# Optimization experiments

Hardware: AMD Instinct MI355X
Metric: run time of the kernel (lower is better)

## Reference

```python
import jax, jax.numpy as jnp
import numpy as np

V, D, H, L, S_MAX, FF = 32000, 1024, 16, 6, 1024, 4096
HD = D // H
EPS = 1e-5

def _ln(x, g, b):
    mu = jnp.mean(x, axis=-1, keepdims=True)
    var = jnp.mean((x - mu) ** 2, axis=-1, keepdims=True)
    return (x - mu) * jax.lax.rsqrt(var + EPS) * g + b

def setup_inputs() -> dict:
    key = jax.random.key(0)
    ks = jax.random.split(key, 12)
    std = 0.02
    d = {}
    d['x'] = jax.random.randint(ks[0], (2, 1024), 0, V)
    d['tok_emb'] = std * jax.random.normal(ks[1], (V, D), jnp.float32)
    d['pos_emb'] = std * jax.random.normal(ks[2], (S_MAX, D), jnp.float32)
    d['ln1_g'] = jnp.ones((L, D)); d['ln1_b'] = jnp.zeros((L, D))
    d['qkv_w'] = std * jax.random.normal(ks[3], (L, 3 * D, D), jnp.float32)
    d['qkv_b'] = jnp.zeros((L, 3 * D))
    d['proj_w'] = std * jax.random.normal(ks[4], (L, D, D), jnp.float32)
    d['proj_b'] = jnp.zeros((L, D))
    d['ln2_g'] = jnp.ones((L, D)); d['ln2_b'] = jnp.zeros((L, D))
    d['fc1_w'] = std * jax.random.normal(ks[5], (L, FF, D), jnp.float32)
    d['fc1_b'] = jnp.zeros((L, FF))
    d['fc2_w'] = std * jax.random.normal(ks[6], (L, D, FF), jnp.float32)
    d['fc2_b'] = jnp.zeros((L, D))
    d['lnf_g'] = jnp.ones((D,)); d['lnf_b'] = jnp.zeros((D,))
    d['head_w'] = std * jax.random.normal(ks[7], (V, D), jnp.float32)
    return d

def _gpt(x, tok_emb, pos_emb, ln1_g, ln1_b, qkv_w, qkv_b, proj_w, proj_b,
         ln2_g, ln2_b, fc1_w, fc1_b, fc2_w, fc2_b, lnf_g, lnf_b, head_w):
    B, S = x.shape
    h = tok_emb[x] + pos_emb[:S][None]  # (B,S,D)
    scale = HD ** -0.5
    causal = jnp.tril(jnp.ones((S, S), bool))
    neg_inf = jnp.finfo(h.dtype).min

    def block(h, p):
        l1g, l1b, qw, qb, pw, pb, l2g, l2b, f1w, f1b, f2w, f2b = p
        xn = _ln(h, l1g, l1b)
        qkv = xn @ qw.T + qb  # (B,S,3D)
        qkv = qkv.reshape(B, S, 3, H, HD).transpose(2, 0, 3, 1, 4)  # (3,B,H,S,HD)
        q, k, v = qkv[0], qkv[1], qkv[2]
        scores = jnp.einsum('bhqd,bhkd->bhqk', q, k) * scale
        scores = jnp.where(causal, scores, neg_inf)
        attn = jax.nn.softmax(scores, axis=-1)
        o = jnp.einsum('bhqk,bhkd->bhqd', attn, v)
        o = o.transpose(0, 2, 1, 3).reshape(B, S, D)
        h = h + (o @ pw.T + pb)
        xn = _ln(h, l2g, l2b)
        ff = jax.nn.gelu(xn @ f1w.T + f1b, approximate=False) @ f2w.T + f2b
        return h + ff, None

    params = (ln1_g, ln1_b, qkv_w, qkv_b, proj_w, proj_b,
              ln2_g, ln2_b, fc1_w, fc1_b, fc2_w, fc2_b)
    h, _ = jax.lax.scan(block, h, params)
    h = _ln(h, lnf_g, lnf_b)
    return h @ head_w.T  # (B,S,V)

def reference(x, tok_emb, pos_emb, ln1_g, ln1_b, qkv_w, qkv_b, proj_w, proj_b,
              ln2_g, ln2_b, fc1_w, fc1_b, fc2_w, fc2_b, lnf_g, lnf_b, head_w):
    return _gpt(x, tok_emb, pos_emb, ln1_g, ln1_b, qkv_w, qkv_b, proj_w, proj_b,
                ln2_g, ln2_b, fc1_w, fc1_b, fc2_w, fc2_b, lnf_g, lnf_b, head_w)
```

## Files before the change

kernel.cpp:

```cpp
#include <hip/hip_runtime.h>

typedef unsigned short u16;
typedef unsigned int   u32;
typedef __bf16 bf16x8 __attribute__((ext_vector_type(8)));
typedef float  f32x4  __attribute__((ext_vector_type(4)));

#define DEV __device__ __forceinline__

DEV u16 f2bf(float f) {
    u32 u = __builtin_bit_cast(u32, f);
    u32 r = u + 0x7FFFu + ((u >> 16) & 1u);
    return (u16)(r >> 16);
}

DEV void gload16(const void* g, void* l) {
    __builtin_amdgcn_global_load_lds((const __attribute__((address_space(1))) void*)g,
                                     (__attribute__((address_space(3))) void*)l, 16, 0, 0);
}

DEV int xcd_swz(int bid, int nwg) {
    int q = nwg >> 3, r = nwg & 7;
    int xcd = bid & 7, idx = bid >> 3;
    return (xcd < r ? xcd * (q + 1) : r * (q + 1) + (xcd - r) * q) + idx;
}

DEV int swz(int p) {
    int m = (((p >> 7) & 1) << 6) | (((p >> 9) & 1) << 5) | (((p >> 8) & 1) << 4);
    return p ^ m;
}

__global__ void cvt_k(const float* __restrict__ src, u16* __restrict__ dst, int n4) {
    int i = blockIdx.x * blockDim.x + threadIdx.x;
    int stride = gridDim.x * blockDim.x;
    for (; i < n4; i += stride) {
        float4 v = ((const float4*)src)[i];
        ushort4 u;
        u.x = f2bf(v.x); u.y = f2bf(v.y); u.z = f2bf(v.z); u.w = f2bf(v.w);
        ((ushort4*)dst)[i] = u;
    }
}

__global__ void cvt4_k(const float* __restrict__ s0, const float* __restrict__ s1,
                       const float* __restrict__ s2, const float* __restrict__ s3,
                       u16* __restrict__ dst, int n0, int n1, int n2, int n3) {
    int i = blockIdx.x * blockDim.x + threadIdx.x;
    int stride = gridDim.x * blockDim.x;
    int t0 = n0, t1 = t0 + n1, t2 = t1 + n2, t3 = t2 + n3;
    for (; i < t3; i += stride) {
        const float* s; int j;
        if (i < t0)      { s = s0; j = i; }
        else if (i < t1) { s = s1; j = i - t0; }
        else if (i < t2) { s = s2; j = i - t1; }
        else             { s = s3; j = i - t2; }
        float4 v = ((const float4*)s)[j];
        ushort4 u;
        u.x = f2bf(v.x); u.y = f2bf(v.y); u.z = f2bf(v.z); u.w = f2bf(v.w);
        ((ushort4*)dst)[i] = u;
    }
}

DEV void ln_store(float4 v, const float* __restrict__ g, const float* __restrict__ b,
                  u16* __restrict__ out, int row, int t) {
    float s = v.x + v.y + v.z + v.w;
    float s2 = v.x * v.x + v.y * v.y + v.z * v.z + v.w * v.w;
    #pragma unroll
    for (int msk = 1; msk < 64; msk <<= 1) {
        s  += __shfl_xor(s, msk);
        s2 += __shfl_xor(s2, msk);
    }
    __shared__ float ps[4], ps2[4];
    if ((t & 63) == 0) { ps[t >> 6] = s; ps2[t >> 6] = s2; }
    __syncthreads();
    s = ps[0] + ps[1] + ps[2] + ps[3];
    s2 = ps2[0] + ps2[1] + ps2[2] + ps2[3];
    float mu = s * (1.0f / 1024.0f);
    float var = s2 * (1.0f / 1024.0f) - mu * mu;
    float rstd = rsqrtf(var + 1e-5f);
    float4 gg = ((const float4*)g)[t];
    float4 bb = ((const float4*)b)[t];
    ushort4 o;
    o.x = f2bf((v.x - mu) * rstd * gg.x + bb.x);
    o.y = f2bf((v.y - mu) * rstd * gg.y + bb.y);
    o.z = f2bf((v.z - mu) * rstd * gg.z + bb.z);
    o.w = f2bf((v.w - mu) * rstd * gg.w + bb.w);
    ((ushort4*)out)[(size_t)row * 256 + t] = o;
}

__global__ void ln_k(const float* __restrict__ in, const float* __restrict__ g,
                     const float* __restrict__ b, u16* __restrict__ out) {
    int row = blockIdx.x;
    int t = threadIdx.x;
    float4 v = ((const float4*)(in + (size_t)row * 1024))[t];
    ln_store(v, g, b, out, row, t);
}

__global__ void embed_ln_k(const int* __restrict__ x, const float* __restrict__ te,
                           const float* __restrict__ pe, float* __restrict__ h,
                           const float* __restrict__ g, const float* __restrict__ b,
                           u16* __restrict__ xn) {
    int row = blockIdx.x;
    int t = threadIdx.x;
    int tok = x[row];
    int s = row & 1023;
    float4 a = ((const float4*)(te + (size_t)tok * 1024))[t];
    float4 p = ((const float4*)(pe + (size_t)s * 1024))[t];
    a.x += p.x; a.y += p.y; a.z += p.z; a.w += p.w;
    ((float4*)(h + (size_t)row * 1024))[t] = a;
    ln_store(a, g, b, xn, row, t);
}

__global__ void fuse2ln_k(const float* __restrict__ p0, const float* __restrict__ p1,
                          const float* __restrict__ bias, float* __restrict__ h,
                          const float* __restrict__ g, const float* __restrict__ b,
                          u16* __restrict__ xn) {
    int row = blockIdx.x;
    int t = threadIdx.x;
    size_t idx = (size_t)row * 256 + t;
    float4 a = ((const float4*)p0)[idx];
    float4 bb = ((const float4*)p1)[idx];
    float4 c = ((const float4*)bias)[t];
    float4 v = ((const float4*)h)[idx];
    v.x += a.x + bb.x + c.x;
    v.y += a.y + bb.y + c.y;
    v.z += a.z + bb.z + c.z;
    v.w += a.w + bb.w + c.w;
    ((float4*)h)[idx] = v;
    ln_store(v, g, b, xn, row, t);
}

template<int PH>
DEV void phase_mma(const bf16x8 (&af)[2][2], const bf16x8 (&bfr)[4][2], f32x4 (&acc)[8][4]) {
    __builtin_amdgcn_s_barrier();
    asm volatile("s_waitcnt lgkmcnt(0)" ::: "memory");
    __builtin_amdgcn_sched_barrier(0);
    __builtin_amdgcn_s_setprio(1);
    #pragma unroll
    for (int ms = 0; ms < 2; ++ms)
        #pragma unroll
        for (int nj = 0; nj < 4; ++nj)
            #pragma unroll
            for (int kk = 0; kk < 2; ++kk)
                acc[PH * 2 + ms][nj] = __builtin_amdgcn_mfma_f32_16x16x32_bf16(
                    af[ms][kk], bfr[nj][kk], acc[PH * 2 + ms][nj], 0, 0, 0);
    __builtin_amdgcn_s_setprio(0);
}

template<int PH>
DEV void read_afrags(const char* Ab, int arow, int fr, int fq, bf16x8 (&af)[2][2]) {
    #pragma unroll
    for (int ms = 0; ms < 2; ++ms)
        #pragma unroll
        for (int kk = 0; kk < 2; ++kk) {
            int lin = (arow + (PH * 2 + ms) * 16 + fr) * 128 + kk * 64 + fq * 16;
            af[ms][kk] = *(const bf16x8*)(Ab + swz(lin));
        }
}

template<int BIAS, int OUTBF>
__global__ __launch_bounds__(512, 2)
void gemm8p(const u16* __restrict__ A, const u16* __restrict__ Bw,
            const float* __restrict__ bias,
            float* __restrict__ outf, u16* __restrict__ outb,
            int M, int N, int K) {
    __shared__ char lds[131072];
    char* ldsA = lds;
    char* ldsB = lds + 65536;
    const int t = threadIdx.x;
    const int w = t >> 6, l = t & 63;
    const int fr = l & 15, fq = l >> 4;
    const int wm = w >> 2, wn = w & 3;

    int bid = blockIdx.y * gridDim.x + blockIdx.x;
    int swzb = xcd_swz(bid, gridDim.x * gridDim.y);
    const int m0 = (swzb % gridDim.x) * 256;
    const int n0 = (swzb / gridDim.x) * 256;
    const int nt = K >> 6;
    const int arow = wm * 128;

    const u16* Asrc = A + (size_t)m0 * K;
    const u16* Bsrc = Bw + (size_t)n0 * K;

    size_t o00, o01, o10, o11;
    {
        int p;
        p = 0 * 16384 + 0 * 8192 + t * 16; o00 = (size_t)(p >> 7) * K + ((swz(p) & 127) >> 1);
        p = 0 * 16384 + 1 * 8192 + t * 16; o01 = (size_t)(p >> 7) * K + ((swz(p) & 127) >> 1);
        p = 1 * 16384 + 0 * 8192 + t * 16; o10 = (size_t)(p >> 7) * K + ((swz(p) & 127) >> 1);
        p = 1 * 16384 + 1 * 8192 + t * 16; o11 = (size_t)(p >> 7) * K + ((swz(p) & 127) >> 1);
    }
    const int wb = w * 1024;

    gload16(Asrc + o00, ldsA + wb);
    gload16(Asrc + o01, ldsA + 8192 + wb);
    gload16(Asrc + o10, ldsA + 16384 + wb);
    gload16(Asrc + o11, ldsA + 16384 + 8192 + wb);
    gload16(Bsrc + o00, ldsB + wb);
    gload16(Bsrc + o01, ldsB + 8192 + wb);
    gload16(Bsrc + o10, ldsB + 16384 + wb);
    gload16(Bsrc + o11, ldsB + 16384 + 8192 + wb);
    gload16(Bsrc + o00 + 64, ldsB + 32768 + wb);
    gload16(Bsrc + o01 + 64, ldsB + 32768 + 8192 + wb);
    gload16(Bsrc + o10 + 64, ldsB + 32768 + 16384 + wb);
    gload16(Bsrc + o11 + 64, ldsB + 32768 + 16384 + 8192 + wb);
    asm volatile("s_waitcnt vmcnt(4)" ::: "memory");
    __builtin_amdgcn_s_barrier();
    __builtin_amdgcn_sched_barrier(0);

    f32x4 acc[8][4] = {};

    for (int T = 0; T < nt; ++T) {
        const char* Ab = ldsA + (T & 1) * 32768;
        const char* Bb = ldsB + (T & 1) * 32768;
        char* Anx = ldsA + ((T + 1) & 1) * 32768;
        char* Bnx = ldsB + (T & 1) * 32768;
        const bool stA = (T + 1 < nt), stB = (T + 2 < nt);
        const size_t kA = (size_t)(T + 1) * 64, kB = (size_t)(T + 2) * 64;

        bf16x8 bfr[4][2], af[2][2];

        #pragma unroll
        for (int nj = 0; nj < 4; ++nj)
            #pragma unroll
            for (int kk = 0; kk < 2; ++kk) {
                int lin = (wn * 64 + nj * 16 + fr) * 128 + kk * 64 + fq * 16;
                bfr[nj][kk] = *(const bf16x8*)(Bb + swz(lin));
            }
        read_afrags<0>(Ab, arow, fr, fq, af);
        if (stA) {
            gload16(Asrc + o00 + kA, Anx + wb);
            gload16(Asrc + o01 + kA, Anx + 8192 + wb);
        }
        phase_mma<0>(af, bfr, acc);
        __builtin_amdgcn_s_barrier();

        read_afrags<1>(Ab, arow, fr, fq, af);
        if (stA) {
            gload16(Asrc + o10 + kA, Anx + 16384 + wb);
            gload16(Asrc + o11 + kA, Anx + 16384 + 8192 + wb);
        }
        phase_mma<1>(af, bfr, acc);
        __builtin_amdgcn_s_barrier();

        read_afrags<2>(Ab, arow, fr, fq, af);
        if (stB) {
            gload16(Bsrc + o00 + kB, Bnx + wb);
            gload16(Bsrc + o01 + kB, Bnx + 8192 + wb);
        }
        phase_mma<2>(af, bfr, acc);
        __builtin_amdgcn_s_barrier();

        read_afrags<3>(Ab, arow, fr, fq, af);
        if (stB) {
            gload16(Bsrc + o10 + kB, Bnx + 16384 + wb);
            gload16(Bsrc + o11 + kB, Bnx + 16384 + 8192 + wb);
        }
        phase_mma<3>(af, bfr, acc);
        if (stB)      asm volatile("s_waitcnt vmcnt(4)" ::: "memory");
        else if (stA) asm volatile("s_waitcnt vmcnt(0)" ::: "memory");
        __builtin_amdgcn_s_barrier();
        __builtin_amdgcn_sched_barrier(0);
    }

    #pragma unroll
    for (int mi = 0; mi < 8; ++mi) {
        #pragma unroll
        for (int nj = 0; nj < 4; ++nj) {
            #pragma unroll
            for (int r = 0; r < 4; ++r) {
                int row = m0 + wm * 128 + mi * 16 + fq * 4 + r;
                int col = n0 + wn * 64 + nj * 16 + fr;
                float v = acc[mi][nj][r];
                if (BIAS) v += bias[col];
                if (OUTBF) outb[(size_t)row * N + col] = f2bf(v);
                else       outf[(size_t)row * N + col] = v;
            }
        }
    }
}

template<int BIAS, int GELU_, int OUTBF, int SPLITK>
__global__ __launch_bounds__(512, 2)
void gemm4p(const u16* __restrict__ A, const u16* __restrict__ Bw,
            const float* __restrict__ bias,
            float* __restrict__ outf, u16* __restrict__ outb,
            int M, int N, int K) {
    __shared__ char lds[65536];
    char* ldsA = lds;
    char* ldsB = lds + 32768;
    const int t = threadIdx.x;
    const int w = t >> 6, l = t & 63;
    const int fr = l & 15, fq = l >> 4;
    const int wm = w >> 2, wn = w & 3;

    int bid = blockIdx.y * gridDim.x + blockIdx.x;
    int swzb = xcd_swz(bid, gridDim.x * gridDim.y);
    const int m0 = (swzb % gridDim.x) * 128;
    const int n0 = (swzb / gridDim.x) * 128;

    int kbase = 0, Keff = K;
    if (SPLITK) { Keff = K >> 1; kbase = blockIdx.z * Keff; }
    const int nt = Keff >> 6;

    const u16* Asrc = A + (size_t)m0 * K + kbase;
    const u16* Bsrc = Bw + (size_t)n0 * K + kbase;

    size_t o0, o1;
    {
        int p = t * 16;        o0 = (size_t)(p >> 7) * K + ((swz(p) & 127) >> 1);
        p = 8192 + t * 16;     o1 = (size_t)(p >> 7) * K + ((swz(p) & 127) >> 1);
    }
    const int wb = w * 1024;

    gload16(Asrc + o0, ldsA + wb);
    gload16(Asrc + o1, ldsA + 8192 + wb);
    gload16(Bsrc + o0, ldsB + wb);
    gload16(Bsrc + o1, ldsB + 8192 + wb);
    gload16(Bsrc + o0 + 64, ldsB + 16384 + wb);
    gload16(Bsrc + o1 + 64, ldsB + 16384 + 8192 + wb);
    asm volatile("s_waitcnt vmcnt(2)" ::: "memory");
    __builtin_amdgcn_s_barrier();
    __builtin_amdgcn_sched_barrier(0);

    f32x4 acc[4][2] = {};

    for (int T = 0; T < nt; ++T) {
        const char* Ab = ldsA + (T & 1) * 16384;
        const char* Bb = ldsB + (T & 1) * 16384;
        char* Anx = ldsA + ((T + 1) & 1) * 16384;
        char* Bnx = ldsB + (T & 1) * 16384;
        const bool stA = (T + 1 < nt), stB = (T + 2 < nt);
        const size_t kA = (size_t)(T + 1) * 64, kB = (size_t)(T + 2) * 64;

        bf16x8 bfr[2][2], af[2][2];

        #pragma unroll
        for (int nj = 0; nj < 2; ++nj)
            #pragma unroll
            for (int kk = 0; kk < 2; ++kk) {
                int lin = (wn * 32 + nj * 16 + fr) * 128 + kk * 64 + fq * 16;
                bfr[nj][kk] = *(const bf16x8*)(Bb + swz(lin));
            }
        #pragma unroll
        for (int ms = 0; ms < 2; ++ms)
            #pragma unroll
            for (int kk = 0; kk < 2; ++kk) {
                int lin = (wm * 64 + ms * 16 + fr) * 128 + kk * 64 + fq * 16;
                af[ms][kk] = *(const bf16x8*)(Ab + swz(lin));
            }
        if (stA) {
            gload16(Asrc + o0 + kA, Anx + wb);
            gload16(Asrc + o1 + kA, Anx + 8192 + wb);
        }
        __builtin_amdgcn_s_barrier();
        asm volatile("s_waitcnt lgkmcnt(0)" ::: "memory");
        __builtin_amdgcn_sched_barrier(0);
        __builtin_amdgcn_s_setprio(1);
        #pragma unroll
        for (int ms = 0; ms < 2; ++ms)
            #pragma unroll
            for (int nj = 0; nj < 2; ++nj)
                #pragma unroll
                for (int kk = 0; kk < 2; ++kk)
                    acc[ms][nj] = __builtin_amdgcn_mfma_f32_16x16x32_bf16(
                        af[ms][kk], bfr[nj][kk], acc[ms][nj], 0, 0, 0);
        __builtin_amdgcn_s_setprio(0);
        __builtin_amdgcn_s_barrier();

        #pragma unroll
        for (int ms = 0; ms < 2; ++ms)
            #pragma unroll
            for (int kk = 0; kk < 2; ++kk) {
                int lin = (wm * 64 + (2 + ms) * 16 + fr) * 128 + kk * 64 + fq * 16;
                af[ms][kk] = *(const bf16x8*)(Ab + swz(lin));
            }
        if (stB) {
            gload16(Bsrc + o0 + kB, Bnx + wb);
            gload16(Bsrc + o1 + kB, Bnx + 8192 + wb);
        }
        __builtin_amdgcn_s_barrier();
        asm volatile("s_waitcnt lgkmcnt(0)" ::: "memory");
        __builtin_amdgcn_sched_barrier(0);
        __builtin_amdgcn_s_setprio(1);
        #pragma unroll
        for (int ms = 0; ms < 2; ++ms)
            #pragma unroll
            for (int nj = 0; nj < 2; ++nj)
                #pragma unroll
                for (int kk = 0; kk < 2; ++kk)
                    acc[2 + ms][nj] = __builtin_amdgcn_mfma_f32_16x16x32_bf16(
                        af[ms][kk], bfr[nj][kk], acc[2 + ms][nj], 0, 0, 0);
        __builtin_amdgcn_s_setprio(0);
        if (stB)      asm volatile("s_waitcnt vmcnt(2)" ::: "memory");
        else if (stA) asm volatile("s_waitcnt vmcnt(0)" ::: "memory");
        __builtin_amdgcn_s_barrier();
        __builtin_amdgcn_sched_barrier(0);
    }

    float* op = outf;
    if (SPLITK) op = outf + (size_t)blockIdx.z * M * N;

    #pragma unroll
    for (int mi = 0; mi < 4; ++mi) {
        #pragma unroll
        for (int nj = 0; nj < 2; ++nj) {
            #pragma unroll
            for (int r = 0; r < 4; ++r) {
                int row = m0 + wm * 64 + mi * 16 + fq * 4 + r;
                int col = n0 + wn * 32 + nj * 16 + fr;
                float v = acc[mi][nj][r];
                if (BIAS) v += bias[col];
                if (GELU_) v = 0.5f * v * (1.0f + erff(v * 0.70710678118f));
                if (OUTBF) outb[(size_t)row * N + col] = f2bf(v);
                else       op[(size_t)row * N + col] = v;
            }
        }
    }
}

template<int BM, int BN, int BIAS, int GELU_, int RES, int OUTBF, int SPLITK>
__global__ void gemm_db(const u16* __restrict__ A, const u16* __restrict__ Bw,
                        const float* __restrict__ bias, const float* __restrict__ res,
                        float* __restrict__ outf, u16* __restrict__ outb,
                        int M, int N, int K) {
    constexpr int MR = BM / 32;
    constexpr int NR = BN / 32;
    constexpr int AL = BM / 64;
    constexpr int BL = BN / 64;
    __shared__ u16 lA[2][BM * 32];
    __shared__ u16 lB[2][BN * 32];
    const int t = threadIdx.x;
    const int w = t >> 6, l = t & 63;

    int bid = blockIdx.y * gridDim.x + blockIdx.x;
    int swzb = xcd_swz(bid, gridDim.x * gridDim.y);
    const int m0 = (swzb % gridDim.x) * BM;
    const int n0 = (swzb / gridDim.x) * BN;

    int kbase = 0, Keff = K;
    if (SPLITK) { Keff = K >> 1; kbase = blockIdx.z * Keff; }
    const int nt = Keff >> 5;

    const int wr = (w >> 1) * (BM / 2), wc = (w & 1) * (BN / 2);
    const int fr = l & 15, fq = l >> 4;
    const int g0 = w * 64 + l;

    const int srow = g0 >> 2, scol = (g0 & 3) * 8;

    f32x4 acc[MR][NR] = {};

    #pragma unroll
    for (int i = 0; i < AL; ++i)
        gload16(A + (size_t)(m0 + srow + i * 64) * K + kbase + scol, lA[0] + (srow + i * 64) * 32 + scol);
    #pragma unroll
    for (int i = 0; i < BL; ++i)
        gload16(Bw + (size_t)(n0 + srow + i * 64) * K + kbase + scol, lB[0] + (srow + i * 64) * 32 + scol);
    __syncthreads();

    for (int T = 0; T < nt; ++T) {
        const int cur = T & 1, nxt = cur ^ 1;
        if (T + 1 < nt) {
            const int kk = kbase + (T + 1) * 32;
            #pragma unroll
            for (int i = 0; i < AL; ++i)
                gload16(A + (size_t)(m0 + srow + i * 64) * K + kk + scol, lA[nxt] + (srow + i * 64) * 32 + scol);
            #pragma unroll
            for (int i = 0; i < BL; ++i)
                gload16(Bw + (size_t)(n0 + srow + i * 64) * K + kk + scol, lB[nxt] + (srow + i * 64) * 32 + scol);
        }
        bf16x8 af[MR], bfv[NR];
        #pragma unroll
        for (int mi = 0; mi < MR; ++mi)
            af[mi] = *(const bf16x8*)(lA[cur] + (wr + mi * 16 + fr) * 32 + fq * 8);
        #pragma unroll
        for (int ni = 0; ni < NR; ++ni)
            bfv[ni] = *(const bf16x8*)(lB[cur] + (wc + ni * 16 + fr) * 32 + fq * 8);
        #pragma unroll
        for (int mi = 0; mi < MR; ++mi)
            #pragma unroll
            for (int ni = 0; ni < NR; ++ni)
                acc[mi][ni] = __builtin_amdgcn_mfma_f32_16x16x32_bf16(af[mi], bfv[ni], acc[mi][ni], 0, 0, 0);
        __syncthreads();
    }

    float* op = outf;
    if (SPLITK) op = outf + (size_t)blockIdx.z * M * N;

    #pragma unroll
    for (int mi = 0; mi < MR; ++mi) {
        #pragma unroll
        for (int ni = 0; ni < NR; ++ni) {
            #pragma unroll
            for (int r = 0; r < 4; ++r) {
                int row = m0 + wr + mi * 16 + fq * 4 + r;
                int col = n0 + wc + ni * 16 + fr;
                float v = acc[mi][ni][r];
                if (BIAS) v += bias[col];
                if (GELU_) v = 0.5f * v * (1.0f + erff(v * 0.70710678118f));
                if (RES) v += res[(size_t)row * N + col];
                if (OUTBF) outb[(size_t)row * N + col] = f2bf(v);
                else       op[(size_t)row * N + col] = v;
            }
        }
    }
}

__global__ __launch_bounds__(512, 2)
void attn_k(const u16* __restrict__ qkv, u16* __restrict__ o) {
    __shared__ u16 lK[2][64 * 64];
    __shared__ u16 lV[2][64 * 64];
    __shared__ u16 lP[8 * 16 * 64];
    const int t = threadIdx.x;
    const int w = t >> 6, l = t & 63;
    const int fr = l & 15, fq = l >> 4;

    int swzb = xcd_swz(blockIdx.x, gridDim.x);
    const int qb = 7 - (swzb & 7);
    const int hh = (swzb >> 3) & 15;
    const int b  = swzb >> 7;
    const int q0 = qb * 128;
    const int qw = q0 + w * 16;

    const u16* srcK;
    {
        int p = t * 16;
        int L = swz(p);
        srcK = qkv + ((size_t)(b * 1024) + (L >> 7)) * 3072 + 1024 + hh * 64 + ((L & 127) >> 1);
    }

    const int kvp = (t & 31) * 2;
    const int vd0 = (t >> 5) * 4;
    const u16* srcV = qkv + (size_t)(b * 1024) * 3072 + 2048 + hh * 64 + vd0;

    bf16x8 qf[2];
    {
        size_t base = ((size_t)(b * 1024) + qw + fr) * 3072 + hh * 64;
        qf[0] = *(const bf16x8*)(qkv + base + fq * 8);
        qf[1] = *(const bf16x8*)(qkv + base + 32 + fq * 8);
    }

    float m_run[4], l_run[4];
    f32x4 acc_o[4] = {};
    #pragma unroll
    for (int r = 0; r < 4; ++r) { m_run[r] = -__builtin_inff(); l_run[r] = 0.0f; }

    uint2 gv0 = *(const uint2*)(srcV + (size_t)kvp * 3072);
    uint2 gv1 = *(const uint2*)(srcV + (size_t)(kvp + 1) * 3072);
    gload16(srcK, (char*)lK[0] + w * 1024);
    #pragma unroll
    for (int j = 0; j < 4; ++j) {
        u32 lo = (j < 2) ? gv0.x : gv0.y;
        u32 hi = (j < 2) ? gv1.x : gv1.y;
        lo = (j & 1) ? (lo >> 16) : (lo & 0xffffu);
        hi = (j & 1) ? (hi >> 16) : (hi & 0xffffu);
        u32 word = lo | (hi << 16);
        int pv = (vd0 + j) * 128 + kvp * 2;
        *(u32*)((char*)lV[0] + swz(pv)) = word;
    }

    const int kv_end = q0 + 128;
    int cur = 0;
    for (int kv0 = 0; kv0 < kv_end; kv0 += 64, cur ^= 1) {
        __syncthreads();
        const int nxt = cur ^ 1;
        const bool more = (kv0 + 64 < kv_end);
        if (more) {
            gload16(srcK + (size_t)(kv0 + 64) * 3072, (char*)lK[nxt] + w * 1024);
            gv0 = *(const uint2*)(srcV + (size_t)(kv0 + 64 + kvp) * 3072);
            gv1 = *(const uint2*)(srcV + (size_t)(kv0 + 64 + kvp + 1) * 3072);
        }

        const bool active = (kv0 <= qw + 15);
        if (active) {
            f32x4 accs[4] = {};
            #pragma unroll
            for (int nt = 0; nt < 4; ++nt) {
                #pragma unroll
                for (int ks = 0; ks < 2; ++ks) {
                    int pk = ((nt * 16 + fr) * 64 + ks * 32 + fq * 8) * 2;
                    bf16x8 kf = *(const bf16x8*)((const char*)lK[cur] + swz(pk));
                    accs[nt] = __builtin_amdgcn_mfma_f32_16x16x32_bf16(qf[ks], kf, accs[nt], 0, 0, 0);
                }
            }

            float p[4][4], mx[4], rs[4];
            #pragma unroll
            for (int r = 0; r < 4; ++r) {
                int qg = qw + fq * 4 + r;
                float m = -__builtin_inff();
                #pragma unroll
                for (int nt = 0; nt < 4; ++nt) {
                    int kvg = kv0 + nt * 16 + fr;
                    float s = (kvg <= qg) ? accs[nt][r] * 0.125f : -__builtin_inff();
                    p[nt][r] = s;
                    m = fmaxf(m, s);
                }
                mx[r] = m;
            }
            #pragma unroll
            for (int msk = 1; msk < 16; msk <<= 1) {
                #pragma unroll
                for (int r = 0; r < 4; ++r) mx[r] = fmaxf(mx[r], __shfl_xor(mx[r], msk));
            }

            bool need = false;
            #pragma unroll
            for (int r = 0; r < 4; ++r) need |= (mx[r] > m_run[r] + 8.0f);
            if (__any(need)) {
                float mnew[4], alpha[4];
                #pragma unroll
                for (int r = 0; r < 4; ++r) {
                    mnew[r] = fmaxf(m_run[r], mx[r]);
                    alpha[r] = __expf(m_run[r] - mnew[r]);
                    float s = 0.0f;
                    #pragma unroll
                    for (int nt = 0; nt < 4; ++nt) {
                        float pv = __expf(p[nt][r] - mnew[r]);
                        p[nt][r] = pv;
                        s += pv;
                    }
                    rs[r] = s;
                }
                #pragma unroll
                for (int msk = 1; msk < 16; msk <<= 1) {
                    #pragma unroll
                    for (int r = 0; r < 4; ++r) rs[r] += __shfl_xor(rs[r], msk);
                }
                #pragma unroll
                for (int r = 0; r < 4; ++r) {
                    l_run[r] = l_run[r] * alpha[r] + rs[r];
                    m_run[r] = mnew[r];
                }
                #pragma unroll
                for (int nt = 0; nt < 4; ++nt)
                    #pragma unroll
                    for (int r = 0; r < 4; ++r) acc_o[nt][r] *= alpha[r];
            } else {
                #pragma unroll
                for (int r = 0; r < 4; ++r) {
                    float s = 0.0f;
                    #pragma unroll
                    for (int nt = 0; nt < 4; ++nt) {
                        float pv = __expf(p[nt][r] - m_run[r]);
                        p[nt][r] = pv;
                        s += pv;
                    }
                    rs[r] = s;
                }
                #pragma unroll
                for (int msk = 1; msk < 16; msk <<= 1) {
                    #pragma unroll
                    for (int r = 0; r < 4; ++r) rs[r] += __shfl_xor(rs[r], msk);
                }
                #pragma unroll
                for (int r = 0; r < 4; ++r) l_run[r] += rs[r];
            }

            #pragma unroll
            for (int nt = 0; nt < 4; ++nt)
                #pragma unroll
                for (int r = 0; r < 4; ++r) {
                    int pp = (w * 1024 + (fq * 4 + r) * 64 + nt * 16 + fr) * 2;
                    *(u16*)((char*)lP + swz(pp)) = f2bf(p[nt][r]);
                }

            bf16x8 pa[2];
            #pragma unroll
            for (int ks = 0; ks < 2; ++ks) {
                int ppr = (w * 1024 + fr * 64 + ks * 32 + fq * 8) * 2;
                pa[ks] = *(const bf16x8*)((const char*)lP + swz(ppr));
            }
            #pragma unroll
            for (int nt = 0; nt < 4; ++nt) {
                #pragma unroll
                for (int ks = 0; ks < 2; ++ks) {
                    int pvr = ((nt * 16 + fr) * 64 + ks * 32 + fq * 8) * 2;
                    bf16x8 vf = *(const bf16x8*)((const char*)lV[cur] + swz(pvr));
                    acc_o[nt] = __builtin_amdgcn_mfma_f32_16x16x32_bf16(pa[ks], vf, acc_o[nt], 0, 0, 0);
                }
            }
        }

        if (more) {
            #pragma unroll
            for (int j = 0; j < 4; ++j) {
                u32 lo = (j < 2) ? gv0.x : gv0.y;
                u32 hi = (j < 2) ? gv1.x : gv1.y;
                lo = (j & 1) ? (lo >> 16) : (lo & 0xffffu);
                hi = (j & 1) ? (hi >> 16) : (hi & 0xffffu);
                u32 word = lo | (hi << 16);
                int pv = (vd0 + j) * 128 + kvp * 2;
                *(u32*)((char*)lV[nxt] + swz(pv)) = word;
            }
        }
    }

    #pragma unroll
    for (int nt = 0; nt < 4; ++nt) {
        #pragma unroll
        for (int r = 0; r < 4; ++r) {
            int qg = qw + fq * 4 + r;
            int d = nt * 16 + fr;
            float ov = acc_o[nt][r] / l_run[r];
            o[((size_t)(b * 1024) + qg) * 1024 + hh * 64 + d] = f2bf(ov);
        }
    }
}

extern "C" void kernel_launch(void* const* d_in, const int* in_sizes, int n_in,
                              void* d_out, int out_size, void* d_ws, size_t ws_size,
                              hipStream_t stream) {
    const int*   x       = (const int*)  d_in[0];
    const float* tok_emb = (const float*)d_in[1];
    const float* pos_emb = (const float*)d_in[2];
    const float* ln1_g   = (const float*)d_in[3];
    const float* ln1_b   = (const float*)d_in[4];
    const float* qkv_w   = (const float*)d_in[5];
    const float* qkv_b   = (const float*)d_in[6];
    const float* proj_w  = (const float*)d_in[7];
    const float* proj_b  = (const float*)d_in[8];
    const float* ln2_g   = (const float*)d_in[9];
    const float* ln2_b   = (const float*)d_in[10];
    const float* fc1_w   = (const float*)d_in[11];
    const float* fc1_b   = (const float*)d_in[12];
    const float* fc2_w   = (const float*)d_in[13];
    const float* fc2_b   = (const float*)d_in[14];
    const float* lnf_g   = (const float*)d_in[15];
    const float* lnf_b   = (const float*)d_in[16];
    const float* head_w  = (const float*)d_in[17];
    float* out = (float*)d_out;

    char* ws = (char*)d_ws;
    float* h   = (float*)(ws + 0);
    u16*   xn  = (u16*)(ws + 8388608);
    u16*   qkv = (u16*)(ws + 12582912);
    u16*   ob  = (u16*)(ws + 25165824);
    u16*   ff  = (u16*)(ws + 29360128);
    u16*   wq  = (u16*)(ws + 46137344);
    float* pbuf = (float*)(ws + 12582912);

    u16* wqkv = wq;
    u16* wproj = wqkv + 3072 * 1024;
    u16* wfc1  = wproj + 1024 * 1024;
    u16* wfc2  = wfc1 + 4096 * 1024;

    const int M = 2048;

    embed_ln_k<<<dim3(2048), 256, 0, stream>>>(x, tok_emb, pos_emb, h, ln1_g, ln1_b, xn);

    for (int lyr = 0; lyr < 6; ++lyr) {
        cvt4_k<<<dim3(2048), 256, 0, stream>>>(
            qkv_w + (size_t)lyr * 3072 * 1024, proj_w + (size_t)lyr * 1024 * 1024,
            fc1_w + (size_t)lyr * 4096 * 1024, fc2_w + (size_t)lyr * 1024 * 4096,
            wq, 3072 * 256, 1024 * 256, 4096 * 256, 4096 * 256);
        gemm4p<1, 0, 1, 0><<<dim3(16, 24), 512, 0, stream>>>(
            xn, wqkv, qkv_b + lyr * 3072, nullptr, qkv, M, 3072, 1024);
        attn_k<<<dim3(256), 512, 0, stream>>>(qkv, ob);
        gemm_db<64, 64, 1, 0, 1, 0, 0><<<dim3(32, 16), 256, 0, stream>>>(
            ob, wproj, proj_b + lyr * 1024, h, h, nullptr, M, 1024, 1024);
        ln_k<<<dim3(2048), 256, 0, stream>>>(h, ln2_g + lyr * 1024, ln2_b + lyr * 1024, xn);
        gemm4p<1, 1, 1, 0><<<dim3(16, 32), 512, 0, stream>>>(
            xn, wfc1, fc1_b + lyr * 4096, nullptr, ff, M, 4096, 1024);
        gemm4p<0, 0, 0, 1><<<dim3(16, 8, 2), 512, 0, stream>>>(
            ff, wfc2, nullptr, pbuf, nullptr, M, 1024, 4096);
        const float* g = (lyr < 5) ? (ln1_g + (lyr + 1) * 1024) : lnf_g;
        const float* b = (lyr < 5) ? (ln1_b + (lyr + 1) * 1024) : lnf_b;
        fuse2ln_k<<<dim3(2048), 256, 0, stream>>>(
            pbuf, pbuf + (size_t)M * 1024, fc2_b + lyr * 1024, h, g, b, xn);
    }

    cvt_k<<<dim3(2048), 256, 0, stream>>>(head_w, wq, 32000 * 1024 / 4);
    gemm8p<0, 0><<<dim3(8, 125), 512, 0, stream>>>(
        xn, wq, nullptr, out, nullptr, M, 32000, 1024);
}
```

Measured before the change: 1.193 ms.

## Halve K tile of LM-head GEMM to 32 to shrink LDS footprint

Rewrites the 256x256 LM-head GEMM kernel to step K by 32 instead of 64, with a new swizzle for 64-byte rows, halving LDS use from 128KB to 64KB. Each iteration now runs in two phases of 16 MFMAs instead of four phases of 8. The smaller LDS footprint may let more workgroups reside per CU, but the kernel now has twice as many iterations and barriers per K and less compute per barrier.

```diff
diff --git a/kernel.cpp b/kernel.cpp
--- a/kernel.cpp
+++ b/kernel.cpp
@@ -26,6 +26,11 @@
 
 DEV int swz(int p) {
     int m = (((p >> 7) & 1) << 6) | (((p >> 9) & 1) << 5) | (((p >> 8) & 1) << 4);
+    return p ^ m;
+}
+
+DEV int swz32(int p) {
+    int m = (((p >> 7) & 1) << 5) | (((p >> 8) & 1) << 4);
     return p ^ m;
 }
 
@@ -128,43 +133,15 @@
     ln_store(v, g, b, xn, row, t);
 }
 
-template<int PH>
-DEV void phase_mma(const bf16x8 (&af)[2][2], const bf16x8 (&bfr)[4][2], f32x4 (&acc)[8][4]) {
-    __builtin_amdgcn_s_barrier();
-    asm volatile("s_waitcnt lgkmcnt(0)" ::: "memory");
-    __builtin_amdgcn_sched_barrier(0);
-    __builtin_amdgcn_s_setprio(1);
-    #pragma unroll
-    for (int ms = 0; ms < 2; ++ms)
-        #pragma unroll
-        for (int nj = 0; nj < 4; ++nj)
-            #pragma unroll
-            for (int kk = 0; kk < 2; ++kk)
-                acc[PH * 2 + ms][nj] = __builtin_amdgcn_mfma_f32_16x16x32_bf16(
-                    af[ms][kk], bfr[nj][kk], acc[PH * 2 + ms][nj], 0, 0, 0);
-    __builtin_amdgcn_s_setprio(0);
-}
-
-template<int PH>
-DEV void read_afrags(const char* Ab, int arow, int fr, int fq, bf16x8 (&af)[2][2]) {
-    #pragma unroll
-    for (int ms = 0; ms < 2; ++ms)
-        #pragma unroll
-        for (int kk = 0; kk < 2; ++kk) {
-            int lin = (arow + (PH * 2 + ms) * 16 + fr) * 128 + kk * 64 + fq * 16;
-            af[ms][kk] = *(const bf16x8*)(Ab + swz(lin));
-        }
-}
-
 template<int BIAS, int OUTBF>
 __global__ __launch_bounds__(512, 2)
-void gemm8p(const u16* __restrict__ A, const u16* __restrict__ Bw,
-            const float* __restrict__ bias,
-            float* __restrict__ outf, u16* __restrict__ outb,
-            int M, int N, int K) {
-    __shared__ char lds[131072];
+void gemm8p32(const u16* __restrict__ A, const u16* __restrict__ Bw,
+              const float* __restrict__ bias,
+              float* __restrict__ outf, u16* __restrict__ outb,
+              int M, int N, int K) {
+    __shared__ char lds[65536];
     char* ldsA = lds;
-    char* ldsB = lds + 65536;
+    char* ldsB = lds + 32768;
     const int t = threadIdx.x;
     const int w = t >> 6, l = t & 63;
     const int fr = l & 15, fq = l >> 4;
@@ -174,88 +151,89 @@
     int swzb = xcd_swz(bid, gridDim.x * gridDim.y);
     const int m0 = (swzb % gridDim.x) * 256;
     const int n0 = (swzb / gridDim.x) * 256;
-    const int nt = K >> 6;
+    const int nt = K >> 5;
     const int arow = wm * 128;
 
     const u16* Asrc = A + (size_t)m0 * K;
     const u16* Bsrc = Bw + (size_t)n0 * K;
 
-    size_t o00, o01, o10, o11;
+    size_t o0, o1;
     {
-        int p;
-        p = 0 * 16384 + 0 * 8192 + t * 16; o00 = (size_t)(p >> 7) * K + ((swz(p) & 127) >> 1);
-        p = 0 * 16384 + 1 * 8192 + t * 16; o01 = (size_t)(p >> 7) * K + ((swz(p) & 127) >> 1);
-        p = 1 * 16384 + 0 * 8192 + t * 16; o10 = (size_t)(p >> 7) * K + ((swz(p) & 127) >> 1);
-        p = 1 * 16384 + 1 * 8192 + t * 16; o11 = (size_t)(p >> 7) * K + ((swz(p) & 127) >> 1);
+        int p = t * 16;        o0 = (size_t)(p >> 6) * K + ((swz32(p) & 63) >> 1);
+        p = 8192 + t * 16;     o1 = (size_t)(p >> 6) * K + ((swz32(p) & 63) >> 1);
     }
     const int wb = w * 1024;
 
-    gload16(Asrc + o00, ldsA + wb);
-    gload16(Asrc + o01, ldsA + 8192 + wb);
-    gload16(Asrc + o10, ldsA + 16384 + wb);
-    gload16(Asrc + o11, ldsA + 16384 + 8192 + wb);
-    gload16(Bsrc + o00, ldsB + wb);
-    gload16(Bsrc + o01, ldsB + 8192 + wb);
-    gload16(Bsrc + o10, ldsB + 16384 + wb);
-    gload16(Bsrc + o11, ldsB + 16384 + 8192 + wb);
-    gload16(Bsrc + o00 + 64, ldsB + 32768 + wb);
-    gload16(Bsrc + o01 + 64, ldsB + 32768 + 8192 + wb);
-    gload16(Bsrc + o10 + 64, ldsB + 32768 + 16384 + wb);
-    gload16(Bsrc + o11 + 64, ldsB + 32768 + 16384 + 8192 + wb);
-    asm volatile("s_waitcnt vmcnt(4)" ::: "memory");
+    gload16(Asrc + o0, ldsA + wb);
+    gload16(Asrc + o1, ldsA + 8192 + wb);
+    gload16(Bsrc + o0, ldsB + wb);
+    gload16(Bsrc + o1, ldsB + 8192 + wb);
+    gload16(Bsrc + o0 + 32, ldsB + 16384 + wb);
+    gload16(Bsrc + o1 + 32, ldsB + 16384 + 8192 + wb);
+    asm volatile("s_waitcnt vmcnt(2)" ::: "memory");
     __builtin_amdgcn_s_barrier();
     __builtin_amdgcn_sched_barrier(0);
 
     f32x4 acc[8][4] = {};
 
     for (int T = 0; T < nt; ++T) {
-        const char* Ab = ldsA + (T & 1) * 32768;
-        const char* Bb = ldsB + (T & 1) * 32768;
-        char* Anx = ldsA + ((T + 1) & 1) * 32768;
-        char* Bnx = ldsB + (T & 1) * 32768;
+        const char* Ab = ldsA + (T & 1) * 16384;
+        const char* Bb = ldsB + (T & 1) * 16384;
+        char* Anx = ldsA + ((T + 1) & 1) * 16384;
+        char* Bnx = ldsB + (T & 1) * 16384;
         const bool stA = (T + 1 < nt), stB = (T + 2 < nt);
-        const size_t kA = (size_t)(T + 1) * 64, kB = (size_t)(T + 2) * 64;
-
-        bf16x8 bfr[4][2], af[2][2];
-
-        #pragma unroll
-        for (int nj = 0; nj < 4; ++nj)
-            #pragma unroll
-            for (int kk = 0; kk < 2; ++kk) {
-                int lin = (wn * 64 + nj * 16 + fr) * 128 + kk * 64 + fq * 16;
-                bfr[nj][kk] = *(const bf16x8*)(Bb + swz(lin));
-            }
-        read_afrags<0>(Ab, arow, fr, fq, af);
+        const size_t kA = (size_t)(T + 1) * 32, kB = (size_t)(T + 2) * 32;
+
+        bf16x8 bfr[4], af[4];
+
+        #pragma unroll
+        for (int nj = 0; nj < 4; ++nj) {
+            int lin = (wn * 64 + nj * 16 + fr) * 64 + fq * 16;
+            bfr[nj] = *(const bf16x8*)(Bb + swz32(lin));
+        }
+        #pragma unroll
+        for (int ms = 0; ms < 4; ++ms) {
+            int lin = (arow + ms * 16 + fr) * 64 + fq * 16;
+            af[ms] = *(const bf16x8*)(Ab + swz32(lin));
+        }
         if (stA) {
-            gload16(Asrc + o00 + kA, Anx + wb);
-            gload16(Asrc + o01 + kA, Anx + 8192 + wb);
-        }
-        phase_mma<0>(af, bfr, acc);
+            gload16(Asrc + o0 + kA, Anx + wb);
+            gload16(Asrc + o1 + kA, Anx + 8192 + wb);
+        }
         __builtin_amdgcn_s_barrier();
-
-        read_afrags<1>(Ab, arow, fr, fq, af);
-        if (stA) {
-            gload16(Asrc + o10 + kA, Anx + 16384 + wb);
-            gload16(Asrc + o11 + kA, Anx + 16384 + 8192 + wb);
-        }
-        phase_mma<1>(af, bfr, acc);
+        asm volatile("s_waitcnt lgkmcnt(0)" ::: "memory");
+        __builtin_amdgcn_sched_barrier(0);
+        __builtin_amdgcn_s_setprio(1);
+        #pragma unroll
+        for (int ms = 0; ms < 4; ++ms)
+            #pragma unroll
+            for (int nj = 0; nj < 4; ++nj)
+                acc[ms][nj] = __builtin_amdgcn_mfma_f32_16x16x32_bf16(
+                    af[ms], bfr[nj], acc[ms][nj], 0, 0, 0);
+        __builtin_amdgcn_s_setprio(0);
         __builtin_amdgcn_s_barrier();
 
-        read_afrags<2>(Ab, arow, fr, fq, af);
+        #pragma unroll
+        for (int ms = 0; ms < 4; ++ms) {
+            int lin = (arow + (4 + ms) * 16 + fr) * 64 + fq * 16;
+            af[ms] = *(const bf16x8*)(Ab + swz32(lin));
+        }
         if (stB) {
-            gload16(Bsrc + o00 + kB, Bnx + wb);
-            gload16(Bsrc + o01 + kB, Bnx + 8192 + wb);
-        }
-        phase_mma<2>(af, bfr, acc);
+            gload16(Bsrc + o0 + kB, Bnx + wb);
+            gload16(Bsrc + o1 + kB, Bnx + 8192 + wb);
+        }
         __builtin_amdgcn_s_barrier();
-
-        read_afrags<3>(Ab, arow, fr, fq, af);
-        if (stB) {
-            gload16(Bsrc + o10 + kB, Bnx + 16384 + wb);
-            gload16(Bsrc + o11 + kB, Bnx + 16384 + 8192 + wb);
-        }
-        phase_mma<3>(af, bfr, acc);
-        if (stB)      asm volatile("s_waitcnt vmcnt(4)" ::: "memory");
+        asm volatile("s_waitcnt lgkmcnt(0)" ::: "memory");
+        __builtin_amdgcn_sched_barrier(0);
+        __builtin_amdgcn_s_setprio(1);
+        #pragma unroll
+        for (int ms = 0; ms < 4; ++ms)
+            #pragma unroll
+            for (int nj = 0; nj < 4; ++nj)
+                acc[4 + ms][nj] = __builtin_amdgcn_mfma_f32_16x16x32_bf16(
+                    af[ms], bfr[nj], acc[4 + ms][nj], 0, 0, 0);
+        __builtin_amdgcn_s_setprio(0);
+        if (stB)      asm volatile("s_waitcnt vmcnt(2)" ::: "memory");
         else if (stA) asm volatile("s_waitcnt vmcnt(0)" ::: "memory");
         __builtin_amdgcn_s_barrier();
         __builtin_amdgcn_sched_barrier(0);
@@ -769,6 +747,6 @@
     }
 
     cvt_k<<<dim3(2048), 256, 0, stream>>>(head_w, wq, 32000 * 1024 / 4);
-    gemm8p<0, 0><<<dim3(8, 125), 512, 0, stream>>>(
+    gemm8p32<0, 0><<<dim3(8, 125), 512, 0, stream>>>(
         xn, wq, nullptr, out, nullptr, M, 32000, 1024);
 }
```

Result: no change. 1.203 ms (+0.8%).
